# Kernel optimization log

Measured on AMD Instinct MI355X. Metric: run time of the kernel, lower is better.

## Reference

```python
import jax, jax.numpy as jnp
import numpy as np

B, C, H, W = 4, 256, 64, 64
CK = C // 8  # query/key channels per OUT_RATIO=8


def setup_inputs() -> dict:
    key = jax.random.key(0)
    ks = jax.random.split(key, 8)
    s_in = 1.0 / np.sqrt(C)
    return {
        "x": jax.random.normal(ks[0], (B, C, H, W), dtype=jnp.float32),
        "Wq": jax.random.uniform(ks[1], (CK, C), jnp.float32, -s_in, s_in),
        "bq": jax.random.uniform(ks[2], (CK,), jnp.float32, -s_in, s_in),
        "Wk": jax.random.uniform(ks[3], (CK, C), jnp.float32, -s_in, s_in),
        "bk": jax.random.uniform(ks[4], (CK,), jnp.float32, -s_in, s_in),
        "Wv": jax.random.uniform(ks[5], (C, C), jnp.float32, -s_in, s_in),
        "bv": jax.random.uniform(ks[6], (C,), jnp.float32, -s_in, s_in),
        "gamma": jnp.zeros((1,), dtype=jnp.float32),
    }


def reference(x, Wq, bq, Wk, bk, Wv, bv, gamma):
    b, c, h, w = x.shape
    n = h * w
    xf = x.reshape(b, c, n)  # [B, C, N]
    # 1x1 convs are channel matmuls
    q = jnp.einsum('oc,bcn->bno', Wq, xf) + bq  # [B, N, CK]
    k = jnp.einsum('oc,bcn->bon', Wk, xf) + bk[None, :, None]  # [B, CK, N]
    v = jnp.einsum('oc,bcn->bon', Wv, xf) + bv[None, :, None]  # [B, C, N]
    energy = jnp.einsum('bno,bom->bnm', q, k)  # [B, N, N], unscaled
    attn = jax.nn.softmax(energy, axis=-1)
    out = jnp.einsum('bcm,bnm->bcn', v, attn)  # [B, C, N]
    out = out.reshape(b, c, h, w)
    return gamma[0] * out + x
```

## Files before the change

### kernel.cpp

```cpp
#include <hip/hip_runtime.h>
#include <math.h>


#define BB 4
#define CC 256
#define NN 4096
#define CKK 32

typedef __attribute__((ext_vector_type(4))) float f32x4;
typedef __attribute__((ext_vector_type(8))) short short8;
typedef __attribute__((ext_vector_type(4))) short short4v;
typedef __attribute__((ext_vector_type(2))) unsigned int u32x2;

static __device__ __forceinline__ ushort f2bf(float f) {
    union { float f; unsigned u; } v; v.f = f;
    unsigned r = v.u + 0x7FFFu + ((v.u >> 16) & 1u);
    return (ushort)(r >> 16);
}
static __device__ __forceinline__ float bf2f(ushort h) {
    union { unsigned u; float f; } v; v.u = ((unsigned)h) << 16;
    return v.f;
}
static __device__ __forceinline__ unsigned pack2(float lo, float hi) {
    return ((unsigned)f2bf(hi) << 16) | (unsigned)f2bf(lo);
}

__global__ __launch_bounds__(256) void pack_w_kernel(
    const float* __restrict__ Wq, const float* __restrict__ bq,
    const float* __restrict__ Wk, const float* __restrict__ bk,
    const float* __restrict__ Wv, const float* __restrict__ bv,
    ushort* __restrict__ Wb, float* __restrict__ bias)
{
    const int o = blockIdx.x;
    const int c = threadIdx.x;
    const float* src; float bsc;
    if (o < 32)      { src = Wq + o * CC;        bsc = bq[o]; }
    else if (o < 64) { src = Wk + (o - 32) * CC; bsc = bk[o - 32]; }
    else             { src = Wv + (o - 64) * CC; bsc = bv[o - 64]; }
    Wb[o * CC + c] = f2bf(src[c]);
    if (c == 0) bias[o] = bsc;
}

__global__ __launch_bounds__(256) void xpose_kernel(
    const float* __restrict__ x, ushort* __restrict__ xT)
{
    __shared__ float t[32][33];
    const int b = blockIdx.z, c0 = blockIdx.y * 32, n0 = blockIdx.x * 32;
    const int tid = threadIdx.x;
    #pragma unroll
    for (int i = 0; i < 4; ++i) {
        int idx = tid + i * 256, rr = idx >> 5, nn = idx & 31;
        t[rr][nn] = x[((size_t)b * CC + c0 + rr) * NN + n0 + nn];
    }
    __syncthreads();
    #pragma unroll
    for (int i = 0; i < 4; ++i) {
        int idx = tid + i * 256, rr = idx >> 5, cc = idx & 31;
        xT[((size_t)b * NN + n0 + rr) * CC + c0 + cc] = f2bf(t[cc][rr]);
    }
}

__global__ __launch_bounds__(256) void qkv_mfma_kernel(
    const ushort* __restrict__ Wb, const float* __restrict__ bias,
    const ushort* __restrict__ xT,
    ushort* __restrict__ Q, ushort* __restrict__ Kt, ushort* __restrict__ V)
{
    const int b = blockIdx.y, n0 = blockIdx.x * 64;
    const int tid = threadIdx.x;
    const int w = tid >> 6, lane = tid & 63, l15 = lane & 15, q = lane >> 4;

    f32x4 acc[5][4];
    #pragma unroll
    for (int c5 = 0; c5 < 5; ++c5)
        #pragma unroll
        for (int nc = 0; nc < 4; ++nc) acc[c5][nc] = (f32x4)0.f;

    #pragma unroll
    for (int ks = 0; ks < 8; ++ks) {
        short8 af[5], bf[4];
        #pragma unroll
        for (int c5 = 0; c5 < 5; ++c5)
            af[c5] = *(const short8*)&Wb[(w * 80 + c5 * 16 + l15) * CC + ks * 32 + q * 8];
        #pragma unroll
        for (int nc = 0; nc < 4; ++nc)
            bf[nc] = *(const short8*)&xT[((size_t)b * NN + n0 + nc * 16 + l15) * CC + ks * 32 + q * 8];
        #pragma unroll
        for (int c5 = 0; c5 < 5; ++c5)
            #pragma unroll
            for (int nc = 0; nc < 4; ++nc)
                acc[c5][nc] = __builtin_amdgcn_mfma_f32_16x16x32_bf16(af[c5], bf[nc], acc[c5][nc], 0, 0, 0);
    }

    #pragma unroll
    for (int c5 = 0; c5 < 5; ++c5) {
        const int o0 = w * 80 + c5 * 16;
        float bia[4];
        #pragma unroll
        for (int r = 0; r < 4; ++r) bia[r] = bias[o0 + q * 4 + r];
        if (o0 >= 64) {
            #pragma unroll
            for (int nc = 0; nc < 4; ++nc)
                #pragma unroll
                for (int r = 0; r < 4; ++r)
                    V[((size_t)b * CC + o0 - 64 + q * 4 + r) * NN + n0 + nc * 16 + l15] =
                        f2bf(acc[c5][nc][r] + bia[r]);
        } else {
            ushort* dst = (o0 < 32) ? Q : Kt;
            const int oo = (o0 & 31) + q * 4;
            #pragma unroll
            for (int nc = 0; nc < 4; ++nc) {
                short4v h;
                #pragma unroll
                for (int r = 0; r < 4; ++r) h[r] = (short)f2bf(acc[c5][nc][r] + bia[r]);
                *(short4v*)&dst[((size_t)b * NN + n0 + nc * 16 + l15) * CKK + oo] = h;
            }
        }
    }
}

__global__ __launch_bounds__(256, 2) void attn_mfma_kernel(
    const ushort* __restrict__ Q, const ushort* __restrict__ K,
    const ushort* __restrict__ V,
    ushort* __restrict__ Op, float* __restrict__ Mp, float* __restrict__ Lp,
    int G, int NSEG)
{
    __shared__ __align__(16) ushort vs[256][40];
    __shared__ __align__(16) ushort ks[32][40];
    __shared__ __align__(16) ushort pb[4][32][40];

    const int id = blockIdx.x;
    const int xcd = id & 7, ix = id >> 3;
    const int b = xcd >> 1;
    int g, row;
    if (G == 4) { g = ((xcd & 1) << 1) | (ix & 1); row = ix >> 1; }
    else        { g = xcd & 1;                     row = ix; }
    const int n0 = row * 128;

    const int tid = threadIdx.x;
    const int w = tid >> 6, lane = tid & 63, l15 = lane & 15, q = lane >> 4;
    const int n0w = n0 + w * 32;

    short8 qB0 = *(const short8*)&Q[((size_t)b * NN + n0w + l15) * CKK + q * 8];
    short8 qB1 = *(const short8*)&Q[((size_t)b * NN + n0w + 16 + l15) * CKK + q * 8];

    f32x4 acc[16][2];
    #pragma unroll
    for (int ci = 0; ci < 16; ++ci) { acc[ci][0] = (f32x4)0.f; acc[ci][1] = (f32x4)0.f; }
    float m_i[2] = {-3.0e38f, -3.0e38f};
    float l_p[2] = {0.f, 0.f};

    const size_t kgb = (size_t)b * NN * CKK;
    const size_t vgb = (size_t)b * CC * NN;
    const int m_start = g * NSEG;
    const int NT = NSEG / 32;

    const int srow = tid >> 2, sseg = tid & 3;

    short8 kreg; short8 vreg[4];
    if (tid < 128)
        kreg = *(const short8*)&K[kgb + (size_t)(m_start + srow) * CKK + sseg * 8];
    #pragma unroll
    for (int i = 0; i < 4; ++i)
        vreg[i] = *(const short8*)&V[vgb + (size_t)(srow + i * 64) * NN + m_start + sseg * 8];
    if (tid < 128) *(short8*)&ks[srow][sseg * 8] = kreg;
    #pragma unroll
    for (int i = 0; i < 4; ++i) *(short8*)&vs[srow + i * 64][sseg * 8] = vreg[i];
    __syncthreads();

    for (int mt = 0; mt < NT; ++mt) {
        const bool more = (mt + 1 < NT);
        const int m0n = m_start + (mt + 1) * 32;

        if (more) {
            if (tid < 128)
                kreg = *(const short8*)&K[kgb + (size_t)(m0n + srow) * CKK + sseg * 8];
            #pragma unroll
            for (int i = 0; i < 4; ++i)
                vreg[i] = *(const short8*)&V[vgb + (size_t)(srow + i * 64) * NN + m0n + sseg * 8];
        }

        short8 kA0 = *(const short8*)&ks[l15][q * 8];
        short8 kA1 = *(const short8*)&ks[16 + l15][q * 8];
        f32x4 s00 = __builtin_amdgcn_mfma_f32_16x16x32_bf16(kA0, qB0, (f32x4)0.f, 0, 0, 0);
        f32x4 s10 = __builtin_amdgcn_mfma_f32_16x16x32_bf16(kA1, qB0, (f32x4)0.f, 0, 0, 0);
        f32x4 s01 = __builtin_amdgcn_mfma_f32_16x16x32_bf16(kA0, qB1, (f32x4)0.f, 0, 0, 0);
        f32x4 s11 = __builtin_amdgcn_mfma_f32_16x16x32_bf16(kA1, qB1, (f32x4)0.f, 0, 0, 0);

        #pragma unroll
        for (int h = 0; h < 2; ++h) {
            const f32x4 slo = h ? s01 : s00;
            const f32x4 shi = h ? s11 : s10;
            float mx = fmaxf(fmaxf(fmaxf(slo[0], slo[1]), fmaxf(slo[2], slo[3])),
                             fmaxf(fmaxf(shi[0], shi[1]), fmaxf(shi[2], shi[3])));
            mx = fmaxf(mx, __shfl_xor(mx, 16));
            mx = fmaxf(mx, __shfl_xor(mx, 32));
            const float mo = m_i[h];
            const bool resc = mx > mo + 8.f;
            const float mn = resc ? mx : mo;
            float p[8];
            #pragma unroll
            for (int r = 0; r < 4; ++r) {
                p[r]     = __expf(slo[r] - mn);
                p[4 + r] = __expf(shi[r] - mn);
            }
            const float sum = ((p[0] + p[1]) + (p[2] + p[3])) +
                              ((p[4] + p[5]) + (p[6] + p[7]));
            float al = 1.f;
            if (resc) { al = __expf(mo - mx); m_i[h] = mx; }
            l_p[h] = l_p[h] * al + sum;
            if (__any(resc)) {
                #pragma unroll
                for (int ci = 0; ci < 16; ++ci) acc[ci][h] *= al;
            }
            const int nn = h * 16 + l15;
            u32x2 wlo, whi;
            wlo[0] = pack2(p[0], p[1]); wlo[1] = pack2(p[2], p[3]);
            whi[0] = pack2(p[4], p[5]); whi[1] = pack2(p[6], p[7]);
            *(u32x2*)&pb[w][nn][q * 4]      = wlo;
            *(u32x2*)&pb[w][nn][16 + q * 4] = whi;
        }

        short8 pB0 = *(const short8*)&pb[w][l15][q * 8];
        short8 pB1 = *(const short8*)&pb[w][16 + l15][q * 8];

        #pragma unroll
        for (int ci = 0; ci < 16; ++ci) {
            short8 vA = *(const short8*)&vs[ci * 16 + l15][q * 8];
            acc[ci][0] = __builtin_amdgcn_mfma_f32_16x16x32_bf16(vA, pB0, acc[ci][0], 0, 0, 0);
            acc[ci][1] = __builtin_amdgcn_mfma_f32_16x16x32_bf16(vA, pB1, acc[ci][1], 0, 0, 0);
        }

        __syncthreads();
        if (more) {
            if (tid < 128) *(short8*)&ks[srow][sseg * 8] = kreg;
            #pragma unroll
            for (int i = 0; i < 4; ++i) *(short8*)&vs[srow + i * 64][sseg * 8] = vreg[i];
        }
        __syncthreads();
    }

    float lfull[2], linv[2];
    #pragma unroll
    for (int h = 0; h < 2; ++h) {
        float l = l_p[h];
        l += __shfl_xor(l, 16);
        l += __shfl_xor(l, 32);
        lfull[h] = l; linv[h] = 1.f / l;
    }
    if (q == 0) {
        #pragma unroll
        for (int h = 0; h < 2; ++h) {
            const size_t idx = (size_t)(g * BB + b) * NN + n0w + h * 16 + l15;
            Mp[idx] = m_i[h];
            Lp[idx] = lfull[h];
        }
    }
    ushort* ob = Op + (size_t)(g * BB + b) * CC * NN;
    #pragma unroll
    for (int ci = 0; ci < 16; ++ci)
        #pragma unroll
        for (int h = 0; h < 2; ++h)
            #pragma unroll
            for (int r = 0; r < 4; ++r)
                ob[(size_t)(ci * 16 + q * 4 + r) * NN + n0w + h * 16 + l15] =
                    f2bf(acc[ci][h][r] * linv[h]);
}

template<int G>
__global__ __launch_bounds__(256) void combine_kernel(
    const ushort* __restrict__ Op, const float* __restrict__ Mp,
    const float* __restrict__ Lp, const float* __restrict__ x,
    const float* __restrict__ gamma, float* __restrict__ out)
{
    const int gid = blockIdx.x * 256 + threadIdx.x;
    const int grp   = gid & (NN / 8 - 1);
    const int rowid = gid >> 9;
    const int b = rowid >> 8;
    const int c = rowid & (CC - 1);
    const int n0 = grp * 8;

    f32x4 mp[G][2], lp[G][2];
    #pragma unroll
    for (int g = 0; g < G; ++g) {
        const size_t base = (size_t)(g * BB + b) * NN + n0;
        mp[g][0] = *(const f32x4*)&Mp[base];
        mp[g][1] = *(const f32x4*)&Mp[base + 4];
        lp[g][0] = *(const f32x4*)&Lp[base];
        lp[g][1] = *(const f32x4*)&Lp[base + 4];
    }
    float wgt[G][8];
    #pragma unroll
    for (int h = 0; h < 2; ++h) {
        #pragma unroll
        for (int j = 0; j < 4; ++j) {
            float M = -3.0e38f;
            #pragma unroll
            for (int g = 0; g < G; ++g) M = fmaxf(M, mp[g][h][j]);
            float ws = 0.f;
            #pragma unroll
            for (int g = 0; g < G; ++g) {
                const float wv = lp[g][h][j] * __expf(mp[g][h][j] - M);
                wgt[g][h * 4 + j] = wv;
                ws += wv;
            }
            const float inv = 1.f / ws;
            #pragma unroll
            for (int g = 0; g < G; ++g) wgt[g][h * 4 + j] *= inv;
        }
    }

    short8 opv[G];
    #pragma unroll
    for (int g = 0; g < G; ++g)
        opv[g] = *(const short8*)&Op[((size_t)(g * BB + b) * CC + c) * NN + n0];

    const size_t xbase = ((size_t)b * CC + c) * NN + n0;
    const f32x4 x0 = *(const f32x4*)&x[xbase];
    const f32x4 x1 = *(const f32x4*)&x[xbase + 4];
    const float gm = gamma[0];

    f32x4 o0, o1;
    #pragma unroll
    for (int j = 0; j < 4; ++j) {
        float a = 0.f, bsum = 0.f;
        #pragma unroll
        for (int g = 0; g < G; ++g) {
            a    += wgt[g][j]     * bf2f((ushort)opv[g][j]);
            bsum += wgt[g][4 + j] * bf2f((ushort)opv[g][4 + j]);
        }
        o0[j] = gm * a + x0[j];
        o1[j] = gm * bsum + x1[j];
    }
    *(f32x4*)&out[xbase]     = o0;
    *(f32x4*)&out[xbase + 4] = o1;
}

extern "C" void kernel_launch(void* const* d_in, const int* in_sizes, int n_in,
                              void* d_out, int out_size, void* d_ws, size_t ws_size,
                              hipStream_t stream) {
    const float* x     = (const float*)d_in[0];
    const float* Wq    = (const float*)d_in[1];
    const float* bq    = (const float*)d_in[2];
    const float* Wk    = (const float*)d_in[3];
    const float* bk    = (const float*)d_in[4];
    const float* Wv    = (const float*)d_in[5];
    const float* bv    = (const float*)d_in[6];
    const float* gamma = (const float*)d_in[7];
    float* out = (float*)d_out;

    char* p = (char*)d_ws;
    ushort* Wb   = (ushort*)(p);
    float*  bias = (float*) (p + 163840);
    ushort* xT   = (ushort*)(p + 165120);
    ushort* Qb   = (ushort*)(p + 8553728);
    ushort* Kb   = (ushort*)(p + 9602304);
    ushort* Vc   = (ushort*)(p + 10650880);
    float*  Mpb  = (float*) (p + 19039488);
    float*  Lpb  = (float*) (p + 19301632);
    ushort* Opb  = (ushort*)(p + 19563776);
    const int G = (ws_size >= (size_t)53118208) ? 4 : 2;

    pack_w_kernel<<<dim3(320), 256, 0, stream>>>(Wq, bq, Wk, bk, Wv, bv, Wb, bias);
    xpose_kernel<<<dim3(NN / 32, CC / 32, BB), 256, 0, stream>>>(x, xT);
    qkv_mfma_kernel<<<dim3(NN / 64, BB), 256, 0, stream>>>(Wb, bias, xT, Qb, Kb, Vc);
    attn_mfma_kernel<<<dim3(128 * G), 256, 0, stream>>>(Qb, Kb, Vc, Opb, Mpb, Lpb, G, NN / G);
    const int cblocks = BB * CC * (NN / 8) / 256;
    if (G == 4)
        combine_kernel<4><<<dim3(cblocks), 256, 0, stream>>>(Opb, Mpb, Lpb, x, gamma, out);
    else
        combine_kernel<2><<<dim3(cblocks), 256, 0, stream>>>(Opb, Mpb, Lpb, x, gamma, out);
}
```

Before: 102.4 us.

## Switch attention kernel to 32x32x16 MFMA with register-resident P and double-buffered V

Rewrites the attention inner loop to use 32x32x16 bf16 MFMAs, so each lane owns one query row and its score fragment already sits in registers in the B-operand layout for the PV product. This drops the per-wave LDS round trip for P and the K tile in LDS; K is now loaded directly from global into registers. V is double-buffered in LDS, which removes one of the two barriers per iteration, and the PV MFMA block runs at raised wave priority. The risks are more register pressure from 16-wide accumulators, which could hurt occupancy at 2 blocks per CU, and uncoalesced direct K loads from global.

```diff
diff --git a/kernel.cpp b/kernel.cpp
--- a/kernel.cpp
+++ b/kernel.cpp
@@ -8,9 +8,9 @@
 #define CKK 32
 
 typedef __attribute__((ext_vector_type(4))) float f32x4;
+typedef __attribute__((ext_vector_type(16))) float f32x16;
 typedef __attribute__((ext_vector_type(8))) short short8;
 typedef __attribute__((ext_vector_type(4))) short short4v;
-typedef __attribute__((ext_vector_type(2))) unsigned int u32x2;
 
 static __device__ __forceinline__ ushort f2bf(float f) {
     union { float f; unsigned u; } v; v.f = f;
@@ -124,9 +124,7 @@
     ushort* __restrict__ Op, float* __restrict__ Mp, float* __restrict__ Lp,
     int G, int NSEG)
 {
-    __shared__ __align__(16) ushort vs[256][40];
-    __shared__ __align__(16) ushort ks[32][40];
-    __shared__ __align__(16) ushort pb[4][32][40];
+    __shared__ __align__(16) ushort vs[2][256][40];
 
     const int id = blockIdx.x;
     const int xcd = id & 7, ix = id >> 3;
@@ -137,17 +135,18 @@
     const int n0 = row * 128;
 
     const int tid = threadIdx.x;
-    const int w = tid >> 6, lane = tid & 63, l15 = lane & 15, q = lane >> 4;
+    const int w = tid >> 6, lane = tid & 63;
+    const int l31 = lane & 31, h2 = lane >> 5;
     const int n0w = n0 + w * 32;
 
-    short8 qB0 = *(const short8*)&Q[((size_t)b * NN + n0w + l15) * CKK + q * 8];
-    short8 qB1 = *(const short8*)&Q[((size_t)b * NN + n0w + 16 + l15) * CKK + q * 8];
-
-    f32x4 acc[16][2];
-    #pragma unroll
-    for (int ci = 0; ci < 16; ++ci) { acc[ci][0] = (f32x4)0.f; acc[ci][1] = (f32x4)0.f; }
-    float m_i[2] = {-3.0e38f, -3.0e38f};
-    float l_p[2] = {0.f, 0.f};
+    const size_t qrow = ((size_t)b * NN + n0w + l31) * CKK;
+    short8 qB0 = *(const short8*)&Q[qrow + h2 * 8];
+    short8 qB1 = *(const short8*)&Q[qrow + 16 + h2 * 8];
+
+    f32x16 acc[8];
+    #pragma unroll
+    for (int cb = 0; cb < 8; ++cb) acc[cb] = (f32x16)0.f;
+    float m_i = -3.0e38f, l_p = 0.f;
 
     const size_t kgb = (size_t)b * NN * CKK;
     const size_t vgb = (size_t)b * CC * NN;
@@ -156,114 +155,93 @@
 
     const int srow = tid >> 2, sseg = tid & 3;
 
-    short8 kreg; short8 vreg[4];
-    if (tid < 128)
-        kreg = *(const short8*)&K[kgb + (size_t)(m_start + srow) * CKK + sseg * 8];
+    short8 kA0 = *(const short8*)&K[kgb + (size_t)(m_start + l31) * CKK + h2 * 8];
+    short8 kA1 = *(const short8*)&K[kgb + (size_t)(m_start + l31) * CKK + 16 + h2 * 8];
+    short8 vreg[4];
     #pragma unroll
     for (int i = 0; i < 4; ++i)
         vreg[i] = *(const short8*)&V[vgb + (size_t)(srow + i * 64) * NN + m_start + sseg * 8];
-    if (tid < 128) *(short8*)&ks[srow][sseg * 8] = kreg;
-    #pragma unroll
-    for (int i = 0; i < 4; ++i) *(short8*)&vs[srow + i * 64][sseg * 8] = vreg[i];
+    #pragma unroll
+    for (int i = 0; i < 4; ++i)
+        *(short8*)&vs[0][srow + i * 64][sseg * 8] = vreg[i];
     __syncthreads();
 
+    int cur = 0;
     for (int mt = 0; mt < NT; ++mt) {
         const bool more = (mt + 1 < NT);
-        const int m0n = m_start + (mt + 1) * 32;
-
-        if (more) {
-            if (tid < 128)
-                kreg = *(const short8*)&K[kgb + (size_t)(m0n + srow) * CKK + sseg * 8];
-            #pragma unroll
-            for (int i = 0; i < 4; ++i)
-                vreg[i] = *(const short8*)&V[vgb + (size_t)(srow + i * 64) * NN + m0n + sseg * 8];
-        }
-
-        short8 kA0 = *(const short8*)&ks[l15][q * 8];
-        short8 kA1 = *(const short8*)&ks[16 + l15][q * 8];
-        f32x4 s00 = __builtin_amdgcn_mfma_f32_16x16x32_bf16(kA0, qB0, (f32x4)0.f, 0, 0, 0);
-        f32x4 s10 = __builtin_amdgcn_mfma_f32_16x16x32_bf16(kA1, qB0, (f32x4)0.f, 0, 0, 0);
-        f32x4 s01 = __builtin_amdgcn_mfma_f32_16x16x32_bf16(kA0, qB1, (f32x4)0.f, 0, 0, 0);
-        f32x4 s11 = __builtin_amdgcn_mfma_f32_16x16x32_bf16(kA1, qB1, (f32x4)0.f, 0, 0, 0);
-
-        #pragma unroll
-        for (int h = 0; h < 2; ++h) {
-            const f32x4 slo = h ? s01 : s00;
-            const f32x4 shi = h ? s11 : s10;
-            float mx = fmaxf(fmaxf(fmaxf(slo[0], slo[1]), fmaxf(slo[2], slo[3])),
-                             fmaxf(fmaxf(shi[0], shi[1]), fmaxf(shi[2], shi[3])));
-            mx = fmaxf(mx, __shfl_xor(mx, 16));
-            mx = fmaxf(mx, __shfl_xor(mx, 32));
-            const float mo = m_i[h];
-            const bool resc = mx > mo + 8.f;
-            const float mn = resc ? mx : mo;
-            float p[8];
-            #pragma unroll
-            for (int r = 0; r < 4; ++r) {
-                p[r]     = __expf(slo[r] - mn);
-                p[4 + r] = __expf(shi[r] - mn);
-            }
-            const float sum = ((p[0] + p[1]) + (p[2] + p[3])) +
-                              ((p[4] + p[5]) + (p[6] + p[7]));
-            float al = 1.f;
-            if (resc) { al = __expf(mo - mx); m_i[h] = mx; }
-            l_p[h] = l_p[h] * al + sum;
-            if (__any(resc)) {
-                #pragma unroll
-                for (int ci = 0; ci < 16; ++ci) acc[ci][h] *= al;
-            }
-            const int nn = h * 16 + l15;
-            u32x2 wlo, whi;
-            wlo[0] = pack2(p[0], p[1]); wlo[1] = pack2(p[2], p[3]);
-            whi[0] = pack2(p[4], p[5]); whi[1] = pack2(p[6], p[7]);
-            *(u32x2*)&pb[w][nn][q * 4]      = wlo;
-            *(u32x2*)&pb[w][nn][16 + q * 4] = whi;
-        }
-
-        short8 pB0 = *(const short8*)&pb[w][l15][q * 8];
-        short8 pB1 = *(const short8*)&pb[w][16 + l15][q * 8];
-
-        #pragma unroll
-        for (int ci = 0; ci < 16; ++ci) {
-            short8 vA = *(const short8*)&vs[ci * 16 + l15][q * 8];
-            acc[ci][0] = __builtin_amdgcn_mfma_f32_16x16x32_bf16(vA, pB0, acc[ci][0], 0, 0, 0);
-            acc[ci][1] = __builtin_amdgcn_mfma_f32_16x16x32_bf16(vA, pB1, acc[ci][1], 0, 0, 0);
-        }
-
+        const int m0n = more ? m_start + (mt + 1) * 32 : m_start;
+
+        f32x16 s = __builtin_amdgcn_mfma_f32_32x32x16_bf16(kA0, qB0, (f32x16)0.f, 0, 0, 0);
+        s = __builtin_amdgcn_mfma_f32_32x32x16_bf16(kA1, qB1, s, 0, 0, 0);
+
+        kA0 = *(const short8*)&K[kgb + (size_t)(m0n + l31) * CKK + h2 * 8];
+        kA1 = *(const short8*)&K[kgb + (size_t)(m0n + l31) * CKK + 16 + h2 * 8];
+        #pragma unroll
+        for (int i = 0; i < 4; ++i)
+            vreg[i] = *(const short8*)&V[vgb + (size_t)(srow + i * 64) * NN + m0n + sseg * 8];
+
+        float mx01 = fmaxf(s[0], s[1]),   mx23 = fmaxf(s[2], s[3]);
+        float mx45 = fmaxf(s[4], s[5]),   mx67 = fmaxf(s[6], s[7]);
+        float mx89 = fmaxf(s[8], s[9]),   mxab = fmaxf(s[10], s[11]);
+        float mxcd = fmaxf(s[12], s[13]), mxef = fmaxf(s[14], s[15]);
+        float mx = fmaxf(fmaxf(fmaxf(mx01, mx23), fmaxf(mx45, mx67)),
+                         fmaxf(fmaxf(mx89, mxab), fmaxf(mxcd, mxef)));
+        mx = fmaxf(mx, __shfl_xor(mx, 32));
+        const bool resc = mx > m_i + 8.f;
+        const float mn = resc ? mx : m_i;
+        const float al = resc ? __expf(m_i - mx) : 1.f;
+        float pp[16];
+        #pragma unroll
+        for (int r = 0; r < 16; ++r) pp[r] = __expf(s[r] - mn);
+        float sum = ((pp[0] + pp[1]) + (pp[2] + pp[3])) + ((pp[4] + pp[5]) + (pp[6] + pp[7]))
+                  + ((pp[8] + pp[9]) + (pp[10] + pp[11])) + ((pp[12] + pp[13]) + (pp[14] + pp[15]));
+        l_p = l_p * al + sum;
+        m_i = mn;
+        if (__any(resc)) {
+            #pragma unroll
+            for (int cb = 0; cb < 8; ++cb) acc[cb] *= al;
+        }
+
+        union { unsigned u[8]; short8 v[2]; } P;
+        #pragma unroll
+        for (int g2 = 0; g2 < 8; ++g2) P.u[g2] = pack2(pp[2 * g2], pp[2 * g2 + 1]);
+
+        __builtin_amdgcn_s_setprio(1);
+        #pragma unroll
+        for (int cb = 0; cb < 8; ++cb) {
+            const ushort* vrow = &vs[cur][cb * 32 + l31][0];
+            union { short4v h[2]; short8 v; } A0, A1;
+            A0.h[0] = *(const short4v*)&vrow[h2 * 4];
+            A0.h[1] = *(const short4v*)&vrow[8 + h2 * 4];
+            A1.h[0] = *(const short4v*)&vrow[16 + h2 * 4];
+            A1.h[1] = *(const short4v*)&vrow[24 + h2 * 4];
+            acc[cb] = __builtin_amdgcn_mfma_f32_32x32x16_bf16(A0.v, P.v[0], acc[cb], 0, 0, 0);
+            acc[cb] = __builtin_amdgcn_mfma_f32_32x32x16_bf16(A1.v, P.v[1], acc[cb], 0, 0, 0);
+        }
+        __builtin_amdgcn_s_setprio(0);
+
+        #pragma unroll
+        for (int i = 0; i < 4; ++i)
+            *(short8*)&vs[cur ^ 1][srow + i * 64][sseg * 8] = vreg[i];
         __syncthreads();
-        if (more) {
-            if (tid < 128) *(short8*)&ks[srow][sseg * 8] = kreg;
-            #pragma unroll
-            for (int i = 0; i < 4; ++i) *(short8*)&vs[srow + i * 64][sseg * 8] = vreg[i];
-        }
-        __syncthreads();
-    }
-
-    float lfull[2], linv[2];
-    #pragma unroll
-    for (int h = 0; h < 2; ++h) {
-        float l = l_p[h];
-        l += __shfl_xor(l, 16);
-        l += __shfl_xor(l, 32);
-        lfull[h] = l; linv[h] = 1.f / l;
-    }
-    if (q == 0) {
-        #pragma unroll
-        for (int h = 0; h < 2; ++h) {
-            const size_t idx = (size_t)(g * BB + b) * NN + n0w + h * 16 + l15;
-            Mp[idx] = m_i[h];
-            Lp[idx] = lfull[h];
-        }
+        cur ^= 1;
+    }
+
+    float l = l_p + __shfl_xor(l_p, 32);
+    const float linv = 1.f / l;
+    if (h2 == 0) {
+        const size_t idx = (size_t)(g * BB + b) * NN + n0w + l31;
+        Mp[idx] = m_i;
+        Lp[idx] = l;
     }
     ushort* ob = Op + (size_t)(g * BB + b) * CC * NN;
     #pragma unroll
-    for (int ci = 0; ci < 16; ++ci)
-        #pragma unroll
-        for (int h = 0; h < 2; ++h)
-            #pragma unroll
-            for (int r = 0; r < 4; ++r)
-                ob[(size_t)(ci * 16 + q * 4 + r) * NN + n0w + h * 16 + l15] =
-                    f2bf(acc[ci][h][r] * linv[h]);
+    for (int cb = 0; cb < 8; ++cb)
+        #pragma unroll
+        for (int r = 0; r < 16; ++r) {
+            const int c = cb * 32 + (r & 3) + 8 * (r >> 2) + 4 * h2;
+            ob[(size_t)c * NN + n0w + l31] = f2bf(acc[cb][r] * linv);
+        }
 }
 
 template<int G>
```

Result: faster. 99.14 us (-3.2%).
